# Kernel optimization log

Hardware: AMD Instinct MI355X
Metric: run time of the kernel (lower is better)

## Reference

```python
import jax, jax.numpy as jnp
import numpy as np
from jax import lax

I, H, B, T = 2048, 96, 64, 512

def _rnn_layer(x_in, w_ih, b_ih, w_hh, b_hh):
    """One tanh-RNN layer. x_in: [B, T, D]. Returns [B, T, H]."""
    # Hoist the big input GEMM out of the scan (one batched matmul).
    xproj = jnp.einsum('btd,hd->bth', x_in, w_ih) + b_ih  # [B, T, H]
    def step(h, xt):  # h: [B, H], xt: [B, H]
        h = jnp.tanh(xt + h @ w_hh.T + b_hh)
        return h, h
    h0 = jnp.zeros((x_in.shape[0], w_hh.shape[0]), dtype=x_in.dtype)
    _, ys = lax.scan(step, h0, jnp.swapaxes(xproj, 0, 1))  # [T, B, H]
    return jnp.swapaxes(ys, 0, 1)

def setup_inputs() -> dict:
    key = jax.random.key(0)
    ks = jax.random.split(key, 12)
    s = 0.05  # keep pre-activations in tanh's linear-ish range
    x = jax.random.normal(ks[0], (B, T, I), dtype=jnp.float32)
    return {
        'x': x,
        'w_ih0': jax.random.normal(ks[1], (H, I), jnp.float32) * s,
        'w_hh0': jax.random.normal(ks[2], (H, H), jnp.float32) * s,
        'b_ih0': jnp.zeros((H,), jnp.float32),
        'b_hh0': jnp.zeros((H,), jnp.float32),
        'w_ih1': jax.random.normal(ks[3], (H, H), jnp.float32) * s,
        'w_hh1': jax.random.normal(ks[4], (H, H), jnp.float32) * s,
        'b_ih1': jnp.zeros((H,), jnp.float32),
        'b_hh1': jnp.zeros((H,), jnp.float32),
        'w_ih2': jax.random.normal(ks[5], (H, H), jnp.float32) * s,
        'w_hh2': jax.random.normal(ks[6], (H, H), jnp.float32) * s,
        'b_ih2': jnp.zeros((H,), jnp.float32),
        'b_hh2': jnp.zeros((H,), jnp.float32),
        'fc_w': jax.random.normal(ks[7], (1, H), jnp.float32) * s,
        'fc_b': jnp.zeros((1,), jnp.float32),
    }

def reference(x, w_ih0, w_hh0, b_ih0, b_hh0,
              w_ih1, w_hh1, b_ih1, b_hh1,
              w_ih2, w_hh2, b_ih2, b_hh2,
              fc_w, fc_b):
    # 3-layer tanh RNN (eval mode: inter-layer dropout p=0.1 and head dropout
    # p=0.2 are identity), then last-timestep linear head.
    h1 = _rnn_layer(x,  w_ih0, b_ih0, w_hh0, b_hh0)  # [B, T, H]
    h2 = _rnn_layer(h1, w_ih1, b_ih1, w_hh1, b_hh1)
    h3 = _rnn_layer(h2, w_ih2, b_ih2, w_hh2, b_hh2)
    last = h3[:, -1, :]                               # [B, H]
    return last @ fc_w.T + fc_b                       # [B, 1]
```

## Files before the change

### kernel.cpp

```cpp
#include <hip/hip_runtime.h>
#include <hip/hip_bf16.h>

#define T_STEPS 512
#define B_SZ 64
#define H_SZ 96
#define I_SZ 2048

#define BM 64
#define BN 96
#define BK 32

typedef const __attribute__((address_space(1))) void g_void;
typedef __attribute__((address_space(3))) void l_void;

__device__ __forceinline__ void stage_tile(const float* __restrict__ x,
                                           const float* __restrict__ w,
                                           float* xsf, float* wsf,
                                           int buf, int m0, int k0, int tid) {
#pragma unroll
    for (int it = 0; it < 2; ++it) {
        int L = tid + it * 256;
        int m = L >> 3;
        int c = (L & 7) ^ ((L >> 5) & 7);
        const float* g = &x[(size_t)(m0 + m) * I_SZ + k0 + c * 4];
        __builtin_amdgcn_global_load_lds((g_void*)g,
            (l_void*)(xsf + buf * (BM * BK) + L * 4), 16, 0, 0);
    }
#pragma unroll
    for (int it = 0; it < 3; ++it) {
        int L = tid + it * 256;
        int j = L >> 3;
        int c = (L & 7) ^ ((L >> 5) & 7);
        const float* g = &w[(size_t)j * I_SZ + k0 + c * 4];
        __builtin_amdgcn_global_load_lds((g_void*)g,
            (l_void*)(wsf + buf * (BN * BK) + L * 4), 16, 0, 0);
    }
}

__global__ __launch_bounds__(256) void xproj_gemm(
    const float* __restrict__ x,
    const float* __restrict__ w,
    const float* __restrict__ bias,
    float* __restrict__ out)
{
    __shared__ __align__(16) float xsf[2 * BM * BK];
    __shared__ __align__(16) float wsf[2 * BN * BK];

    const int tid = threadIdx.x;
    const int m0 = blockIdx.x * BM;
    const int tm = tid & 15;
    const int tn = tid >> 4;

    float bb[6];
#pragma unroll
    for (int c = 0; c < 6; ++c) bb[c] = bias[tn * 6 + c];

    int aoff[4], boff[6], sb[6];
    const int sa = tm & 7;
#pragma unroll
    for (int r = 0; r < 4; ++r) aoff[r] = (tm * 4 + r) * 8;
#pragma unroll
    for (int c = 0; c < 6; ++c) {
        int j = tn * 6 + c;
        boff[c] = j * 8;
        sb[c] = (j >> 2) & 7;
    }

    float acc[4][6];
#pragma unroll
    for (int r = 0; r < 4; ++r)
#pragma unroll
        for (int c = 0; c < 6; ++c) acc[r][c] = 0.f;

    stage_tile(x, w, xsf, wsf, 0, m0, 0, tid);
    __syncthreads();

    for (int tile = 0; tile < I_SZ / BK; ++tile) {
        const int buf = tile & 1;
        if (tile < I_SZ / BK - 1)
            stage_tile(x, w, xsf, wsf, buf ^ 1, m0, (tile + 1) * BK, tid);

        const float4* xsb = (const float4*)(xsf + buf * (BM * BK));
        const float4* wsb = (const float4*)(wsf + buf * (BN * BK));
#pragma unroll
        for (int cc = 0; cc < 8; ++cc) {
            float av[4][4], bv[6][4];
#pragma unroll
            for (int r = 0; r < 4; ++r)
                *(float4*)av[r] = xsb[aoff[r] + (cc ^ sa)];
#pragma unroll
            for (int c = 0; c < 6; ++c)
                *(float4*)bv[c] = wsb[boff[c] + (cc ^ sb[c])];
#pragma unroll
            for (int kk = 0; kk < 4; ++kk)
#pragma unroll
                for (int r = 0; r < 4; ++r)
#pragma unroll
                    for (int c = 0; c < 6; ++c)
                        acc[r][c] = fmaf(av[r][kk], bv[c][kk], acc[r][c]);
        }
        __syncthreads();
    }

#pragma unroll
    for (int r = 0; r < 4; ++r) {
        float* op = &out[(size_t)(m0 + tm * 4 + r) * H_SZ + tn * 6];
        *(float2*)(op + 0) = make_float2(acc[r][0] + bb[0], acc[r][1] + bb[1]);
        *(float2*)(op + 2) = make_float2(acc[r][2] + bb[2], acc[r][3] + bb[3]);
        *(float2*)(op + 4) = make_float2(acc[r][4] + bb[4], acc[r][5] + bb[5]);
    }
}


#define PP 8
#define RING 32
#define NCH (T_STEPS / PP)
#define NPER (NCH + 4)

__device__ __forceinline__ float fast_tanh(float x) {
    float cx = fminf(fmaxf(x, -15.f), 15.f);
    float e = __expf(2.f * cx);
    return 1.f - 2.f / (e + 1.f);
}

__device__ __forceinline__ void serial_chunk(
    const float4 (&W)[36], float cb0, float cb1, float cb2,
    float* ringS, const float* ihsrc, int tb, int p, int kh)
{
    const int j0 = 3 * p;
    const int hbase = kh * 48;
#pragma unroll
    for (int i8 = 0; i8 < PP; ++i8) {
        const int tt = tb + i8;
        const float* hp = &ringS[((tt - 1) & (RING - 1)) * H_SZ + hbase];
        const float* ih = &ihsrc[i8 * H_SZ + j0];
        float id0 = ih[0], id1 = ih[1], id2 = ih[2];
        float a0x = 0.f, a0y = 0.f, a0z = 0.f, a0w = 0.f;
        float a1x = 0.f, a1y = 0.f, a1z = 0.f, a1w = 0.f;
        float a2x = 0.f, a2y = 0.f, a2z = 0.f, a2w = 0.f;
#pragma unroll
        for (int c = 0; c < 12; ++c) {
            float4 h = *(const float4*)(hp + c * 4);
            a0x = fmaf(W[c].x,      h.x, a0x); a0y = fmaf(W[c].y,      h.y, a0y);
            a0z = fmaf(W[c].z,      h.z, a0z); a0w = fmaf(W[c].w,      h.w, a0w);
            a1x = fmaf(W[12 + c].x, h.x, a1x); a1y = fmaf(W[12 + c].y, h.y, a1y);
            a1z = fmaf(W[12 + c].z, h.z, a1z); a1w = fmaf(W[12 + c].w, h.w, a1w);
            a2x = fmaf(W[24 + c].x, h.x, a2x); a2y = fmaf(W[24 + c].y, h.y, a2y);
            a2z = fmaf(W[24 + c].z, h.z, a2z); a2w = fmaf(W[24 + c].w, h.w, a2w);
        }
        float a0 = (a0x + a0y) + (a0z + a0w);
        float a1 = (a1x + a1y) + (a1z + a1w);
        float a2 = (a2x + a2y) + (a2z + a2w);
        a0 += __shfl_xor(a0, 1, 64);
        a1 += __shfl_xor(a1, 1, 64);
        a2 += __shfl_xor(a2, 1, 64);
        float h0v = fast_tanh(a0 + id0 + cb0);
        float h1v = fast_tanh(a1 + id1 + cb1);
        float h2v = fast_tanh(a2 + id2 + cb2);
        const int so = (tt & (RING - 1)) * H_SZ;
        if (kh == 0) {
            ringS[so + j0 + 0] = h0v;
            ringS[so + j0 + 1] = h1v;
        } else {
            ringS[so + j0 + 2] = h2v;
        }
    }
}

__device__ __forceinline__ void bulk_chunk(
    const float4 (&W)[24], const float* ringSrc,
    float* dst, int tb, int row, bool act)
{
#pragma unroll
    for (int i8 = 0; i8 < PP; ++i8) {
        const float* hp = &ringSrc[((tb + i8) & (RING - 1)) * H_SZ];
        float ax = 0.f, ay = 0.f, az = 0.f, aw = 0.f;
#pragma unroll
        for (int c = 0; c < 24; ++c) {
            float4 h = *(const float4*)(hp + c * 4);
            ax = fmaf(W[c].x, h.x, ax); ay = fmaf(W[c].y, h.y, ay);
            az = fmaf(W[c].z, h.z, az); aw = fmaf(W[c].w, h.w, aw);
        }
        if (act) dst[i8 * H_SZ + row] = (ax + ay) + (az + aw);
    }
}

__global__ __launch_bounds__(512, 2) void rnn3_fused(
    const float* __restrict__ xproj0,
    const float* __restrict__ w_hh0, const float* __restrict__ b_hh0,
    const float* __restrict__ w_ih1, const float* __restrict__ b_ih1,
    const float* __restrict__ w_hh1, const float* __restrict__ b_hh1,
    const float* __restrict__ w_ih2, const float* __restrict__ b_ih2,
    const float* __restrict__ w_hh2, const float* __restrict__ b_hh2,
    const float* __restrict__ fc_w, const float* __restrict__ fc_b,
    float* __restrict__ out)
{
    __shared__ __align__(16) float ring0[RING * H_SZ];
    __shared__ __align__(16) float ring1[RING * H_SZ];
    __shared__ __align__(16) float ring2[RING * H_SZ];
    __shared__ __align__(16) float ihd1[2][PP * H_SZ];
    __shared__ __align__(16) float ihd2[2][PP * H_SZ];
    __shared__ __align__(16) float xpb[2][PP * H_SZ];
    __shared__ float red[H_SZ];

    const int t = threadIdx.x;
    const int b = blockIdx.x;
    const int wv = t >> 6;
    const int l = t & 63;

    for (int k = t; k < RING * H_SZ; k += 512) {
        ring0[k] = 0.f; ring1[k] = 0.f; ring2[k] = 0.f;
    }

    const float* xp_base = xproj0 + (size_t)b * T_STEPS * H_SZ;

    if (wv == 5) {
#pragma unroll
        for (int q = 0; q < 3; ++q) {
            int idx = (l + 64 * q) * 4;
            *(float4*)&xpb[0][idx] = *(const float4*)&xp_base[idx];
        }
    }
    __syncthreads();

    if (wv < 3) {
        const int p = l >> 1, kh = l & 1, j0 = 3 * p;
        const float* wm = (wv == 0) ? w_hh0 : (wv == 1 ? w_hh1 : w_hh2);
        float4 W[36];
#pragma unroll
        for (int r = 0; r < 3; ++r)
#pragma unroll
            for (int c = 0; c < 12; ++c)
                W[r * 12 + c] = *(const float4*)&wm[(j0 + r) * H_SZ + kh * 48 + c * 4];
        float cb0, cb1, cb2;
        if (wv == 0) {
            cb0 = b_hh0[j0]; cb1 = b_hh0[j0 + 1]; cb2 = b_hh0[j0 + 2];
        } else if (wv == 1) {
            cb0 = b_ih1[j0]     + b_hh1[j0];
            cb1 = b_ih1[j0 + 1] + b_hh1[j0 + 1];
            cb2 = b_ih1[j0 + 2] + b_hh1[j0 + 2];
        } else {
            cb0 = b_ih2[j0]     + b_hh2[j0];
            cb1 = b_ih2[j0 + 1] + b_hh2[j0 + 1];
            cb2 = b_ih2[j0 + 2] + b_hh2[j0 + 2];
        }
        float* ringS = (wv == 0) ? ring0 : (wv == 1 ? ring1 : ring2);
        __builtin_amdgcn_s_setprio(1);
        for (int m = 0; m < NPER; ++m) {
            const int cc = m - 2 * wv;
            if (cc >= 0 && cc < NCH) {
                const float* ihsrc = (wv == 0) ? &xpb[m & 1][0]
                                   : (wv == 1) ? &ihd1[cc & 1][0]
                                               : &ihd2[cc & 1][0];
                serial_chunk(W, cb0, cb1, cb2, ringS, ihsrc, cc * PP, p, kh);
            }
            __syncthreads();
        }
        __builtin_amdgcn_s_setprio(0);
    } else if (wv == 3 || wv == 4) {
        const int rr = (wv - 3) * 64 + l;
        const bool rowact = rr < H_SZ;
        const int rowid = rowact ? rr : (H_SZ - 1);
        float4 W[24];
#pragma unroll
        for (int c = 0; c < 24; ++c)
            W[c] = *(const float4*)&w_ih1[rowid * H_SZ + c * 4];
        for (int m = 0; m < NPER; ++m) {
            const int cc = m - 1;
            if (cc >= 0 && cc < NCH)
                bulk_chunk(W, ring0, &ihd1[cc & 1][0], cc * PP, rowid, rowact);
            __syncthreads();
        }
    } else if (wv == 5) {
        for (int m = 0; m < NPER; ++m) {
            const int cs = m + 1;
            if (cs < NCH) {
                const float* src = xp_base + (size_t)cs * PP * H_SZ;
                float* dstx = &xpb[cs & 1][0];
#pragma unroll
                for (int q = 0; q < 3; ++q) {
                    int idx = (l + 64 * q) * 4;
                    *(float4*)&dstx[idx] = *(const float4*)&src[idx];
                }
            }
            __syncthreads();
        }
    } else {
        const int rr = (wv - 6) * 64 + l;
        const bool rowact = rr < H_SZ;
        const int rowid = rowact ? rr : (H_SZ - 1);
        float4 W[24];
#pragma unroll
        for (int c = 0; c < 24; ++c)
            W[c] = *(const float4*)&w_ih2[rowid * H_SZ + c * 4];
        for (int m = 0; m < NPER; ++m) {
            const int cc = m - 3;
            if (cc >= 0 && cc < NCH)
                bulk_chunk(W, ring1, &ihd2[cc & 1][0], cc * PP, rowid, rowact);
            __syncthreads();
        }
    }
    __syncthreads();

    if (t < H_SZ) red[t] = ring2[((T_STEPS - 1) & (RING - 1)) * H_SZ + t] * fc_w[t];
    __syncthreads();
    if (t == 0) {
        float sm = 0.f;
#pragma unroll
        for (int k = 0; k < H_SZ; ++k) sm += red[k];
        out[b] = sm + fc_b[0];
    }
}

extern "C" void kernel_launch(void* const* d_in, const int* in_sizes, int n_in,
                              void* d_out, int out_size, void* d_ws, size_t ws_size,
                              hipStream_t stream) {
    const float* x     = (const float*)d_in[0];
    const float* w_ih0 = (const float*)d_in[1];
    const float* w_hh0 = (const float*)d_in[2];
    const float* b_ih0 = (const float*)d_in[3];
    const float* b_hh0 = (const float*)d_in[4];
    const float* w_ih1 = (const float*)d_in[5];
    const float* w_hh1 = (const float*)d_in[6];
    const float* b_ih1 = (const float*)d_in[7];
    const float* b_hh1 = (const float*)d_in[8];
    const float* w_ih2 = (const float*)d_in[9];
    const float* w_hh2 = (const float*)d_in[10];
    const float* b_ih2 = (const float*)d_in[11];
    const float* b_hh2 = (const float*)d_in[12];
    const float* fc_w  = (const float*)d_in[13];
    const float* fc_b  = (const float*)d_in[14];

    float* xproj = (float*)d_ws;

    const int M = B_SZ * T_STEPS;
    xproj_gemm<<<M / BM, 256, 0, stream>>>(x, w_ih0, b_ih0, xproj);
    rnn3_fused<<<B_SZ, 512, 0, stream>>>(xproj,
                                         w_hh0, b_hh0,
                                         w_ih1, b_ih1, w_hh1, b_hh1,
                                         w_ih2, b_ih2, w_hh2, b_hh2,
                                         fc_w, fc_b, (float*)d_out);
}
```

Measured before the change: 858.2 us.

## Compute inter-layer input projections with one wave each, shrinking block to 384 threads

The inter-layer input projections (w_ih1, w_ih2) were each computed by two waves, one row per lane, with half of the second wave idle. They now use one wave per layer with the same 3-row, half-K split and shuffle reduction as the serial recurrence waves, and the block drops from 8 to 6 waves. The aim is to remove the idle lanes and cut the number of waves taking part in every per-chunk __syncthreads barrier. In exchange, each projection wave now does twice the work per chunk and uses more registers (36 float4 weights), which could put it on the critical path of the pipeline. The trailing extra barrier before the final reduction is also removed.

```diff
diff --git a/kernel.cpp b/kernel.cpp
--- a/kernel.cpp
+++ b/kernel.cpp
@@ -167,25 +167,46 @@
     }
 }
 
-__device__ __forceinline__ void bulk_chunk(
-    const float4 (&W)[24], const float* ringSrc,
-    float* dst, int tb, int row, bool act)
+__device__ __forceinline__ void ih_chunk(
+    const float4 (&W)[36], const float* ringSrc,
+    float* dst, int tb, int p, int kh)
 {
+    const int j0 = 3 * p;
+    const int hbase = kh * 48;
 #pragma unroll
     for (int i8 = 0; i8 < PP; ++i8) {
-        const float* hp = &ringSrc[((tb + i8) & (RING - 1)) * H_SZ];
-        float ax = 0.f, ay = 0.f, az = 0.f, aw = 0.f;
-#pragma unroll
-        for (int c = 0; c < 24; ++c) {
+        const int tt = tb + i8;
+        const float* hp = &ringSrc[(tt & (RING - 1)) * H_SZ + hbase];
+        float a0x = 0.f, a0y = 0.f, a0z = 0.f, a0w = 0.f;
+        float a1x = 0.f, a1y = 0.f, a1z = 0.f, a1w = 0.f;
+        float a2x = 0.f, a2y = 0.f, a2z = 0.f, a2w = 0.f;
+#pragma unroll
+        for (int c = 0; c < 12; ++c) {
             float4 h = *(const float4*)(hp + c * 4);
-            ax = fmaf(W[c].x, h.x, ax); ay = fmaf(W[c].y, h.y, ay);
-            az = fmaf(W[c].z, h.z, az); aw = fmaf(W[c].w, h.w, aw);
-        }
-        if (act) dst[i8 * H_SZ + row] = (ax + ay) + (az + aw);
-    }
-}
-
-__global__ __launch_bounds__(512, 2) void rnn3_fused(
+            a0x = fmaf(W[c].x,      h.x, a0x); a0y = fmaf(W[c].y,      h.y, a0y);
+            a0z = fmaf(W[c].z,      h.z, a0z); a0w = fmaf(W[c].w,      h.w, a0w);
+            a1x = fmaf(W[12 + c].x, h.x, a1x); a1y = fmaf(W[12 + c].y, h.y, a1y);
+            a1z = fmaf(W[12 + c].z, h.z, a1z); a1w = fmaf(W[12 + c].w, h.w, a1w);
+            a2x = fmaf(W[24 + c].x, h.x, a2x); a2y = fmaf(W[24 + c].y, h.y, a2y);
+            a2z = fmaf(W[24 + c].z, h.z, a2z); a2w = fmaf(W[24 + c].w, h.w, a2w);
+        }
+        float a0 = (a0x + a0y) + (a0z + a0w);
+        float a1 = (a1x + a1y) + (a1z + a1w);
+        float a2 = (a2x + a2y) + (a2z + a2w);
+        a0 += __shfl_xor(a0, 1, 64);
+        a1 += __shfl_xor(a1, 1, 64);
+        a2 += __shfl_xor(a2, 1, 64);
+        float* dp = &dst[i8 * H_SZ + j0];
+        if (kh == 0) {
+            dp[0] = a0;
+            dp[1] = a1;
+        } else {
+            dp[2] = a2;
+        }
+    }
+}
+
+__global__ __launch_bounds__(384, 2) void rnn3_fused(
     const float* __restrict__ xproj0,
     const float* __restrict__ w_hh0, const float* __restrict__ b_hh0,
     const float* __restrict__ w_ih1, const float* __restrict__ b_ih1,
@@ -207,8 +228,9 @@
     const int b = blockIdx.x;
     const int wv = t >> 6;
     const int l = t & 63;
-
-    for (int k = t; k < RING * H_SZ; k += 512) {
+    const int p = l >> 1, kh = l & 1, j0 = 3 * p;
+
+    for (int k = t; k < RING * H_SZ; k += 384) {
         ring0[k] = 0.f; ring1[k] = 0.f; ring2[k] = 0.f;
     }
 
@@ -224,7 +246,6 @@
     __syncthreads();
 
     if (wv < 3) {
-        const int p = l >> 1, kh = l & 1, j0 = 3 * p;
         const float* wm = (wv == 0) ? w_hh0 : (wv == 1 ? w_hh1 : w_hh2);
         float4 W[36];
 #pragma unroll
@@ -257,21 +278,33 @@
             __syncthreads();
         }
         __builtin_amdgcn_s_setprio(0);
-    } else if (wv == 3 || wv == 4) {
-        const int rr = (wv - 3) * 64 + l;
-        const bool rowact = rr < H_SZ;
-        const int rowid = rowact ? rr : (H_SZ - 1);
-        float4 W[24];
-#pragma unroll
-        for (int c = 0; c < 24; ++c)
-            W[c] = *(const float4*)&w_ih1[rowid * H_SZ + c * 4];
+    } else if (wv == 3) {
+        float4 W[36];
+#pragma unroll
+        for (int r = 0; r < 3; ++r)
+#pragma unroll
+            for (int c = 0; c < 12; ++c)
+                W[r * 12 + c] = *(const float4*)&w_ih1[(j0 + r) * H_SZ + kh * 48 + c * 4];
         for (int m = 0; m < NPER; ++m) {
             const int cc = m - 1;
             if (cc >= 0 && cc < NCH)
-                bulk_chunk(W, ring0, &ihd1[cc & 1][0], cc * PP, rowid, rowact);
+                ih_chunk(W, ring0, &ihd1[cc & 1][0], cc * PP, p, kh);
             __syncthreads();
         }
-    } else if (wv == 5) {
+    } else if (wv == 4) {
+        float4 W[36];
+#pragma unroll
+        for (int r = 0; r < 3; ++r)
+#pragma unroll
+            for (int c = 0; c < 12; ++c)
+                W[r * 12 + c] = *(const float4*)&w_ih2[(j0 + r) * H_SZ + kh * 48 + c * 4];
+        for (int m = 0; m < NPER; ++m) {
+            const int cc = m - 3;
+            if (cc >= 0 && cc < NCH)
+                ih_chunk(W, ring1, &ihd2[cc & 1][0], cc * PP, p, kh);
+            __syncthreads();
+        }
+    } else {
         for (int m = 0; m < NPER; ++m) {
             const int cs = m + 1;
             if (cs < NCH) {
@@ -285,22 +318,7 @@
             }
             __syncthreads();
         }
-    } else {
-        const int rr = (wv - 6) * 64 + l;
-        const bool rowact = rr < H_SZ;
-        const int rowid = rowact ? rr : (H_SZ - 1);
-        float4 W[24];
-#pragma unroll
-        for (int c = 0; c < 24; ++c)
-            W[c] = *(const float4*)&w_ih2[rowid * H_SZ + c * 4];
-        for (int m = 0; m < NPER; ++m) {
-            const int cc = m - 3;
-            if (cc >= 0 && cc < NCH)
-                bulk_chunk(W, ring1, &ihd2[cc & 1][0], cc * PP, rowid, rowact);
-            __syncthreads();
-        }
-    }
-    __syncthreads();
+    }
 
     if (t < H_SZ) red[t] = ring2[((T_STEPS - 1) & (RING - 1)) * H_SZ + t] * fc_w[t];
     __syncthreads();
@@ -335,7 +353,7 @@
 
     const int M = B_SZ * T_STEPS;
     xproj_gemm<<<M / BM, 256, 0, stream>>>(x, w_ih0, b_ih0, xproj);
-    rnn3_fused<<<B_SZ, 512, 0, stream>>>(xproj,
+    rnn3_fused<<<B_SZ, 384, 0, stream>>>(xproj,
                                          w_hh0, b_hh0,
                                          w_ih1, b_ih1, w_hh1, b_hh1,
                                          w_ih2, b_ih2, w_hh2, b_hh2,
```

After: 840.0 us. 1.02x faster.

## Restructure xproj GEMM to read weights via wave-uniform scalar loads

Applied to the files above, without the earlier changes.

Rewrites the input-projection GEMM to use 512 threads (8 waves) where each wave owns 12 output columns and each lane owns one row. Only the x tile is staged in LDS; weights are read directly from global memory with wave-uniform addresses, which the compiler can serve through scalar loads and the cache. This removes the LDS weight tile and its bandwidth, but cuts per-thread register reuse from a 4x6 outer product to 1x12, so each LDS float4 now feeds 48 FMAs instead of 96.

```diff
diff --git a/kernel.cpp b/kernel.cpp
--- a/kernel.cpp
+++ b/kernel.cpp
@@ -6,108 +6,73 @@
 #define H_SZ 96
 #define I_SZ 2048
 
-#define BM 64
-#define BN 96
-#define BK 32
+#define GBM 64
+#define GBK 32
 
 typedef const __attribute__((address_space(1))) void g_void;
 typedef __attribute__((address_space(3))) void l_void;
 
-__device__ __forceinline__ void stage_tile(const float* __restrict__ x,
-                                           const float* __restrict__ w,
-                                           float* xsf, float* wsf,
-                                           int buf, int m0, int k0, int tid) {
-#pragma unroll
-    for (int it = 0; it < 2; ++it) {
-        int L = tid + it * 256;
-        int m = L >> 3;
-        int c = (L & 7) ^ ((L >> 5) & 7);
-        const float* g = &x[(size_t)(m0 + m) * I_SZ + k0 + c * 4];
-        __builtin_amdgcn_global_load_lds((g_void*)g,
-            (l_void*)(xsf + buf * (BM * BK) + L * 4), 16, 0, 0);
-    }
-#pragma unroll
-    for (int it = 0; it < 3; ++it) {
-        int L = tid + it * 256;
-        int j = L >> 3;
-        int c = (L & 7) ^ ((L >> 5) & 7);
-        const float* g = &w[(size_t)j * I_SZ + k0 + c * 4];
-        __builtin_amdgcn_global_load_lds((g_void*)g,
-            (l_void*)(wsf + buf * (BN * BK) + L * 4), 16, 0, 0);
-    }
-}
-
-__global__ __launch_bounds__(256) void xproj_gemm(
+__global__ __launch_bounds__(512) void xproj_gemm(
     const float* __restrict__ x,
     const float* __restrict__ w,
     const float* __restrict__ bias,
     float* __restrict__ out)
 {
-    __shared__ __align__(16) float xsf[2 * BM * BK];
-    __shared__ __align__(16) float wsf[2 * BN * BK];
+    __shared__ __align__(16) float xs[2 * GBM * GBK];
 
     const int tid = threadIdx.x;
-    const int m0 = blockIdx.x * BM;
-    const int tm = tid & 15;
-    const int tn = tid >> 4;
-
-    float bb[6];
-#pragma unroll
-    for (int c = 0; c < 6; ++c) bb[c] = bias[tn * 6 + c];
-
-    int aoff[4], boff[6], sb[6];
-    const int sa = tm & 7;
-#pragma unroll
-    for (int r = 0; r < 4; ++r) aoff[r] = (tm * 4 + r) * 8;
-#pragma unroll
-    for (int c = 0; c < 6; ++c) {
-        int j = tn * 6 + c;
-        boff[c] = j * 8;
-        sb[c] = (j >> 2) & 7;
-    }
-
-    float acc[4][6];
-#pragma unroll
-    for (int r = 0; r < 4; ++r)
-#pragma unroll
-        for (int c = 0; c < 6; ++c) acc[r][c] = 0.f;
-
-    stage_tile(x, w, xsf, wsf, 0, m0, 0, tid);
+    const int m0 = blockIdx.x * GBM;
+    const int l = tid & 63;
+    const int wid = __builtin_amdgcn_readfirstlane(tid >> 6);
+    const int j0 = wid * 12;
+
+    const int sm = tid >> 3;
+    const int sc = (tid & 7) ^ ((tid >> 5) & 7);
+
+    float acc[12];
+#pragma unroll
+    for (int j = 0; j < 12; ++j) acc[j] = 0.f;
+
+    const int key = (l >> 2) & 7;
+
+    __builtin_amdgcn_global_load_lds(
+        (g_void*)&x[(size_t)(m0 + sm) * I_SZ + sc * 4],
+        (l_void*)(xs + tid * 4), 16, 0, 0);
     __syncthreads();
 
-    for (int tile = 0; tile < I_SZ / BK; ++tile) {
+    for (int tile = 0; tile < I_SZ / GBK; ++tile) {
         const int buf = tile & 1;
-        if (tile < I_SZ / BK - 1)
-            stage_tile(x, w, xsf, wsf, buf ^ 1, m0, (tile + 1) * BK, tid);
-
-        const float4* xsb = (const float4*)(xsf + buf * (BM * BK));
-        const float4* wsb = (const float4*)(wsf + buf * (BN * BK));
+        if (tile < I_SZ / GBK - 1)
+            __builtin_amdgcn_global_load_lds(
+                (g_void*)&x[(size_t)(m0 + sm) * I_SZ + (tile + 1) * GBK + sc * 4],
+                (l_void*)(xs + (buf ^ 1) * (GBM * GBK) + tid * 4), 16, 0, 0);
+
+        const float* xb = xs + buf * (GBM * GBK) + l * GBK;
+        const float* wt = w + tile * GBK;
 #pragma unroll
         for (int cc = 0; cc < 8; ++cc) {
-            float av[4][4], bv[6][4];
-#pragma unroll
-            for (int r = 0; r < 4; ++r)
-                *(float4*)av[r] = xsb[aoff[r] + (cc ^ sa)];
-#pragma unroll
-            for (int c = 0; c < 6; ++c)
-                *(float4*)bv[c] = wsb[boff[c] + (cc ^ sb[c])];
-#pragma unroll
-            for (int kk = 0; kk < 4; ++kk)
-#pragma unroll
-                for (int r = 0; r < 4; ++r)
-#pragma unroll
-                    for (int c = 0; c < 6; ++c)
-                        acc[r][c] = fmaf(av[r][kk], bv[c][kk], acc[r][c]);
+            float4 av = *(const float4*)(xb + ((cc ^ key) * 4));
+#pragma unroll
+            for (int j = 0; j < 12; ++j) {
+                float4 wv = *(const float4*)(wt + (size_t)(j0 + j) * I_SZ + cc * 4);
+                acc[j] = fmaf(wv.x, av.x, acc[j]);
+                acc[j] = fmaf(wv.y, av.y, acc[j]);
+                acc[j] = fmaf(wv.z, av.z, acc[j]);
+                acc[j] = fmaf(wv.w, av.w, acc[j]);
+            }
         }
         __syncthreads();
     }
 
-#pragma unroll
-    for (int r = 0; r < 4; ++r) {
-        float* op = &out[(size_t)(m0 + tm * 4 + r) * H_SZ + tn * 6];
-        *(float2*)(op + 0) = make_float2(acc[r][0] + bb[0], acc[r][1] + bb[1]);
-        *(float2*)(op + 2) = make_float2(acc[r][2] + bb[2], acc[r][3] + bb[3]);
-        *(float2*)(op + 4) = make_float2(acc[r][4] + bb[4], acc[r][5] + bb[5]);
+    float* op = &out[(size_t)(m0 + l) * H_SZ + j0];
+#pragma unroll
+    for (int q = 0; q < 3; ++q) {
+        float4 v;
+        v.x = acc[q * 4 + 0] + bias[j0 + q * 4 + 0];
+        v.y = acc[q * 4 + 1] + bias[j0 + q * 4 + 1];
+        v.z = acc[q * 4 + 2] + bias[j0 + q * 4 + 2];
+        v.w = acc[q * 4 + 3] + bias[j0 + q * 4 + 3];
+        *(float4*)(op + q * 4) = v;
     }
 }
 
@@ -334,7 +299,7 @@
     float* xproj = (float*)d_ws;
 
     const int M = B_SZ * T_STEPS;
-    xproj_gemm<<<M / BM, 256, 0, stream>>>(x, w_ih0, b_ih0, xproj);
+    xproj_gemm<<<M / GBM, 512, 0, stream>>>(x, w_ih0, b_ih0, xproj);
     rnn3_fused<<<B_SZ, 512, 0, stream>>>(xproj,
                                          w_hh0, b_hh0,
                                          w_ih1, b_ih1, w_hh1, b_hh1,
```

Measured after the change: 1.097 ms. +27.9%, slower.
